# Optimization experiments

Measured on AMD Instinct MI355X. Metric: run time of the kernel, lower is better.

The kernel has to match this reference:

```python
import jax, jax.numpy as jnp
import numpy as np

B, S, DIN = 4, 2048, 1024
H, D = 16, 64  # num_head, per-head dim_out


def _xavier(key, shape):
    fan_in, fan_out = shape[0], shape[1]
    limit = float(np.sqrt(6.0 / (fan_in + fan_out)))
    return jax.random.uniform(key, shape, jnp.float32, -limit, limit)


def setup_inputs() -> dict:
    key = jax.random.key(0)
    k_x, k_q, k_k, k_v, k_o = jax.random.split(key, 5)
    inputs = jax.random.normal(k_x, (B, S, DIN), jnp.float32)
    # weights stored as [in, out] (transpose of torch Linear.weight); bias zeros
    return {
        "inputs": inputs,
        "wq": _xavier(k_q, (DIN, H * D)), "bq": jnp.zeros((H * D,), jnp.float32),
        "wk": _xavier(k_k, (DIN, H * D)), "bk": jnp.zeros((H * D,), jnp.float32),
        "wv": _xavier(k_v, (DIN, H * D)), "bv": jnp.zeros((H * D,), jnp.float32),
        "wo": _xavier(k_o, (H * D, D)),  "bo": jnp.zeros((D,), jnp.float32),
    }


def reference(inputs, wq, bq, wk, bk, wv, bv, wo, bo):
    b, s, _ = inputs.shape
    q = (inputs @ wq + bq).reshape(b, s, H, D).transpose(0, 2, 1, 3)  # bhsd
    k = (inputs @ wk + bk).reshape(b, s, H, D).transpose(0, 2, 1, 3)
    v = (inputs @ wv + bv).reshape(b, s, H, D).transpose(0, 2, 1, 3)
    scores = jnp.einsum('bhsd,bhSd->bhsS', q, k) / jnp.sqrt(jnp.float32(D))
    p = jax.nn.softmax(scores, axis=-1)
    o = jnp.einsum('bhsS,bhSd->bhsd', p, v)
    o = o.transpose(0, 2, 1, 3).reshape(b, s, H * D)
    return o @ wo + bo  # [b, s, D]
```

## Files before the change

kernel.cpp:

```cpp
#include <hip/hip_runtime.h>

typedef __attribute__((ext_vector_type(8))) __bf16 bf16x8;
typedef __attribute__((ext_vector_type(4))) float f32x4;

#define NB   4
#define NS   2048
#define NDIN 1024
#define NH   16
#define ND   64
#define NHD  1024
#define NM   (NB * NS)

__device__ __forceinline__ float bf2f(unsigned short u) {
    unsigned int x = ((unsigned int)u) << 16;
    return __builtin_bit_cast(float, x);
}
__device__ __forceinline__ unsigned short f2bf(float f) {
    unsigned int u = __builtin_bit_cast(unsigned int, f);
    u += 0x7fff + ((u >> 16) & 1);
    return (unsigned short)(u >> 16);
}
__device__ __forceinline__ unsigned int cvt_pk_bf16(float lo, float hi) {
    unsigned int r;
    asm("v_cvt_pk_bf16_f32 %0, %1, %2" : "=v"(r) : "v"(lo), "v"(hi));
    return r;
}
__device__ __forceinline__ void gload16(const unsigned short* g, unsigned short* l) {
    __builtin_amdgcn_global_load_lds((const __attribute__((address_space(1))) unsigned int*)g,
                                     (__attribute__((address_space(3))) unsigned int*)l, 16, 0, 0);
}

__global__ __launch_bounds__(256) void cvt_x(const float* __restrict__ src,
                                             unsigned short* __restrict__ dst) {
    int i = blockIdx.x * 256 + threadIdx.x;
    float4 a = ((const float4*)src)[i * 2];
    float4 b = ((const float4*)src)[i * 2 + 1];
    union { uint4 u; unsigned short s[8]; } o;
    o.s[0] = f2bf(a.x); o.s[1] = f2bf(a.y); o.s[2] = f2bf(a.z); o.s[3] = f2bf(a.w);
    o.s[4] = f2bf(b.x); o.s[5] = f2bf(b.y); o.s[6] = f2bf(b.z); o.s[7] = f2bf(b.w);
    *(uint4*)(dst + (size_t)i * 8) = o.u;
}

__global__ void transpose_cvt3(const float* __restrict__ wq, const float* __restrict__ wk,
                               const float* __restrict__ wv, unsigned short* __restrict__ dst_all) {
    __shared__ unsigned short t[32][33];
    const float* src = blockIdx.z == 0 ? wq : blockIdx.z == 1 ? wk : wv;
    unsigned short* dst = dst_all + (size_t)blockIdx.z * 1024 * 1024;
    int k0 = blockIdx.x * 32, n0 = blockIdx.y * 32;
    int tx = threadIdx.x, ty = threadIdx.y;
#pragma unroll
    for (int i = 0; i < 32; i += 8)
        t[ty + i][tx] = f2bf(src[(size_t)(k0 + ty + i) * 1024 + (n0 + tx)]);
    __syncthreads();
#pragma unroll
    for (int i = 0; i < 32; i += 8)
        dst[(size_t)(n0 + ty + i) * 1024 + (k0 + tx)] = t[tx][ty + i];
}

__global__ void transpose_cvt(const float* __restrict__ src,
                              unsigned short* __restrict__ dst, int K, int N) {
    __shared__ unsigned short t[32][33];
    int k0 = blockIdx.x * 32, n0 = blockIdx.y * 32;
    int tx = threadIdx.x, ty = threadIdx.y;
#pragma unroll
    for (int i = 0; i < 32; i += 8)
        t[ty + i][tx] = f2bf(src[(size_t)(k0 + ty + i) * N + (n0 + tx)]);
    __syncthreads();
#pragma unroll
    for (int i = 0; i < 32; i += 8)
        dst[(size_t)(n0 + ty + i) * K + (k0 + tx)] = t[tx][ty + i];
}

__global__ __launch_bounds__(256) void gemm_qkv(
    const unsigned short* __restrict__ X, const unsigned short* __restrict__ Wt,
    const float* __restrict__ bq, const float* __restrict__ bk,
    const float* __restrict__ bv,
    unsigned short* __restrict__ Q, unsigned short* __restrict__ K,
    unsigned short* __restrict__ V) {
    __shared__ unsigned short smem[128 * 128];
    unsigned short (*Al)[32] = (unsigned short (*)[32])smem;
    unsigned short (*Bl)[32] = (unsigned short (*)[32])(smem + 128 * 32);
    unsigned short (*Cl)[128] = (unsigned short (*)[128])smem;

    int lin = blockIdx.x;
    int xcd = lin & 7, ii = lin >> 3;
    int mt = xcd * 8 + (ii & 7);
    int nt = ii >> 3;
    int mb = mt * 128, nb = nt * 128;

    int tid = threadIdx.x;
    int wid = tid >> 6, lane = tid & 63, quad = lane >> 4, l16 = lane & 15;
    int wm = (wid & 1) * 64, wn = (wid >> 1) * 64;

    int srow = 16 * wid + (lane >> 2);
    int scol = (lane & 3) * 8;
    const unsigned short* pa0 = X + (size_t)(mb + srow) * NDIN + scol;
    const unsigned short* pa1 = pa0 + (size_t)64 * NDIN;
    const unsigned short* pb0 = Wt + (size_t)(nb + srow) * NDIN + scol;
    const unsigned short* pb1 = pb0 + (size_t)64 * NDIN;
    unsigned short* la = smem + wid * 512;
    unsigned short* lb = smem + 128 * 32 + wid * 512;

    f32x4 acc[4][4];
#pragma unroll
    for (int i = 0; i < 4; i++)
#pragma unroll
        for (int j = 0; j < 4; j++) acc[i][j] = (f32x4){0.f, 0.f, 0.f, 0.f};

    for (int k0 = 0; k0 < NDIN; k0 += 32) {
        gload16(pa0, la);
        gload16(pa1, la + 2048);
        gload16(pb0, lb);
        gload16(pb1, lb + 2048);
        pa0 += 32; pa1 += 32; pb0 += 32; pb1 += 32;
        __syncthreads();
        bf16x8 af[4], bfr[4];
#pragma unroll
        for (int i = 0; i < 4; i++)
            af[i] = *(const bf16x8*)(&Al[wm + i * 16 + l16][quad * 8]);
#pragma unroll
        for (int j = 0; j < 4; j++)
            bfr[j] = *(const bf16x8*)(&Bl[wn + j * 16 + l16][quad * 8]);
#pragma unroll
        for (int i = 0; i < 4; i++)
#pragma unroll
            for (int j = 0; j < 4; j++)
                acc[i][j] = __builtin_amdgcn_mfma_f32_16x16x32_bf16(af[i], bfr[j], acc[i][j], 0, 0, 0);
        __syncthreads();
    }

    int wsel = nb >> 10;
    const float* bias = (wsel == 0) ? bq : (wsel == 1) ? bk : bv;
    unsigned short* dstp = (wsel == 0) ? Q : (wsel == 1) ? K : V;
#pragma unroll
    for (int i = 0; i < 4; i++)
#pragma unroll
        for (int j = 0; j < 4; j++) {
            int nl = wn + j * 16 + l16;
            float bias_v = bias[(nb & 1023) + nl];
#pragma unroll
            for (int r = 0; r < 4; r++) {
                int ml = wm + i * 16 + quad * 4 + r;
                int pc = ((nl >> 3) ^ (ml & 15));
                Cl[ml][(pc << 3) | (nl & 7)] = f2bf(acc[i][j][r] + bias_v);
            }
        }
    __syncthreads();
    {
        int hl = tid >> 7, sl = tid & 127;
        int h = ((nb & 1023) >> 6) + hl;
        int m = mb + sl, b = m >> 11, sidx = m & 2047;
        unsigned short* orow = dstp + ((size_t)((b * NH + h) * NS + sidx)) * ND;
#pragma unroll
        for (int c = 0; c < 8; c++) {
            int pc = ((hl * 8 + c) ^ (sl & 15));
            *(uint4*)(orow + c * 8) = *(const uint4*)(&Cl[sl][pc << 3]);
        }
    }
}

__global__ __launch_bounds__(256) void attn(
    const unsigned short* __restrict__ Q, const unsigned short* __restrict__ K,
    const unsigned short* __restrict__ V, unsigned short* __restrict__ Obuf) {
    __shared__ unsigned short Kl[2][64][64];
    __shared__ unsigned short Vt[2][64][64];

    int lin = blockIdx.x;
    int xcd = lin & 7, idx = lin >> 3;
    int bh = ((idx >> 4) << 3) | xcd;
    int qt = idx & 15;

    size_t base = (size_t)bh * NS * ND;
    int tid = threadIdx.x, wid = tid >> 6, lane = tid & 63;
    int quad = lane >> 4, l16 = lane & 15;
    int lx = l16 & 7;
    int q0 = qt * 128 + wid * 32;

    bf16x8 qa[2][2];
#pragma unroll
    for (int s = 0; s < 2; s++)
#pragma unroll
        for (int f = 0; f < 2; f++) {
            union { uint4 u; unsigned short sv[8]; } in_, out_;
            in_.u = *(const uint4*)(Q + base + (size_t)(q0 + s * 16 + l16) * ND + f * 32 + quad * 8);
#pragma unroll
            for (int j = 0; j < 8; j++) out_.sv[j] = f2bf(bf2f(in_.sv[j]) * 0.125f);
            qa[s][f] = __builtin_bit_cast(bf16x8, out_.u);
        }

    float lrow[2] = {0.f, 0.f};
    f32x4 o[2][4];
#pragma unroll
    for (int s = 0; s < 2; s++)
#pragma unroll
        for (int t = 0; t < 4; t++) o[s][t] = (f32x4){0.f, 0.f, 0.f, 0.f};

    int c0 = tid, c1 = tid + 256;
    int kr0w = c0 >> 3, kc0 = c0 & 7, kg0c = kc0 ^ (kr0w & 7);
    int kr1w = c1 >> 3, kc1 = c1 & 7, kg1c = kc1 ^ (kr1w & 7);
    const unsigned short* kp0 = K + base + (size_t)kr0w * ND + kc0 * 8;
    const unsigned short* kp1 = K + base + (size_t)kr1w * ND + kc1 * 8;
    int p = tid & 31, dqA = tid >> 5, dqB = dqA + 8;
    int cp = ((p >> 4) << 2) | ((p >> 1) & 3);
    int ps = (((p >> 3) & 1) << 2) | ((p & 1) << 1);
    int cb = cp ^ ((dqA & 1) << 2);
    const unsigned short* vg = V + base + (size_t)(2 * p) * ND + dqA * 4;

    uint4 k0r, k1r;
    uint2 va0, va1, va2, va3;

    auto writeKV = [&](int buf) {
        *(uint4*)(&Kl[buf][kr0w][kg0c * 8]) = k0r;
        *(uint4*)(&Kl[buf][kr1w][kg1c * 8]) = k1r;
        unsigned short* vt = &Vt[buf][0][0];
        unsigned int w0 = __builtin_amdgcn_perm(va1.x, va0.x, 0x05040100u);
        unsigned int w1 = __builtin_amdgcn_perm(va1.x, va0.x, 0x07060302u);
        unsigned int w2 = __builtin_amdgcn_perm(va1.y, va0.y, 0x05040100u);
        unsigned int w3 = __builtin_amdgcn_perm(va1.y, va0.y, 0x07060302u);
        *(unsigned int*)(vt + (dqA * 4 + 0) * 64 + ((cb ^ 0) << 3) + ps) = w0;
        *(unsigned int*)(vt + (dqA * 4 + 1) * 64 + ((cb ^ 1) << 3) + ps) = w1;
        *(unsigned int*)(vt + (dqA * 4 + 2) * 64 + ((cb ^ 2) << 3) + ps) = w2;
        *(unsigned int*)(vt + (dqA * 4 + 3) * 64 + ((cb ^ 3) << 3) + ps) = w3;
        unsigned int x0 = __builtin_amdgcn_perm(va3.x, va2.x, 0x05040100u);
        unsigned int x1 = __builtin_amdgcn_perm(va3.x, va2.x, 0x07060302u);
        unsigned int x2 = __builtin_amdgcn_perm(va3.y, va2.y, 0x05040100u);
        unsigned int x3 = __builtin_amdgcn_perm(va3.y, va2.y, 0x07060302u);
        *(unsigned int*)(vt + (dqB * 4 + 0) * 64 + ((cb ^ 0) << 3) + ps) = x0;
        *(unsigned int*)(vt + (dqB * 4 + 1) * 64 + ((cb ^ 1) << 3) + ps) = x1;
        *(unsigned int*)(vt + (dqB * 4 + 2) * 64 + ((cb ^ 2) << 3) + ps) = x2;
        *(unsigned int*)(vt + (dqB * 4 + 3) * 64 + ((cb ^ 3) << 3) + ps) = x3;
    };

    k0r = *(const uint4*)kp0;
    k1r = *(const uint4*)kp1;
    va0 = *(const uint2*)(vg);
    va1 = *(const uint2*)(vg + ND);
    va2 = *(const uint2*)(vg + 32);
    va3 = *(const uint2*)(vg + ND + 32);
    writeKV(0);
    __syncthreads();

    int cur = 0;
    for (int kc = 0; kc < NS; kc += 64) {
        bool more = (kc + 64 < NS);
        if (more) {
            kp0 += 64 * ND; kp1 += 64 * ND; vg += 64 * ND;
            k0r = *(const uint4*)kp0;
            k1r = *(const uint4*)kp1;
            va0 = *(const uint2*)(vg);
            va1 = *(const uint2*)(vg + ND);
            va2 = *(const uint2*)(vg + 32);
            va3 = *(const uint2*)(vg + ND + 32);
        }

        const unsigned short (*Kc)[64] = Kl[cur];
        const unsigned short (*Vc)[64] = Vt[cur];

        f32x4 st[2][4];
        __builtin_amdgcn_s_setprio(1);
#pragma unroll
        for (int sub = 0; sub < 4; sub++) {
            bf16x8 kb0 = *(const bf16x8*)(&Kc[sub * 16 + l16][((quad ^ lx) << 3)]);
            bf16x8 kb1 = *(const bf16x8*)(&Kc[sub * 16 + l16][(((4 + quad) ^ lx) << 3)]);
#pragma unroll
            for (int s = 0; s < 2; s++) {
                f32x4 c = (f32x4){0.f, 0.f, 0.f, 0.f};
                c = __builtin_amdgcn_mfma_f32_16x16x32_bf16(kb0, qa[s][0], c, 0, 0, 0);
                c = __builtin_amdgcn_mfma_f32_16x16x32_bf16(kb1, qa[s][1], c, 0, 0, 0);
                st[s][sub] = c;
            }
        }
        __builtin_amdgcn_s_setprio(0);

        bf16x8 pb[2][2];
#pragma unroll
        for (int s = 0; s < 2; s++) {
            float sum = 0.f;
#pragma unroll
            for (int sub = 0; sub < 4; sub++)
#pragma unroll
                for (int r = 0; r < 4; r++) {
                    float pv = __expf(st[s][sub][r]);
                    st[s][sub][r] = pv;
                    sum += pv;
                }
            lrow[s] += sum;
            unsigned int a0 = cvt_pk_bf16(st[s][0][0], st[s][0][1]);
            unsigned int a1 = cvt_pk_bf16(st[s][0][2], st[s][0][3]);
            unsigned int a2 = cvt_pk_bf16(st[s][1][0], st[s][1][1]);
            unsigned int a3 = cvt_pk_bf16(st[s][1][2], st[s][1][3]);
            pb[s][0] = __builtin_bit_cast(bf16x8, (uint4){a0, a1, a2, a3});
            unsigned int b0 = cvt_pk_bf16(st[s][2][0], st[s][2][1]);
            unsigned int b1 = cvt_pk_bf16(st[s][2][2], st[s][2][3]);
            unsigned int b2 = cvt_pk_bf16(st[s][3][0], st[s][3][1]);
            unsigned int b3 = cvt_pk_bf16(st[s][3][2], st[s][3][3]);
            pb[s][1] = __builtin_bit_cast(bf16x8, (uint4){b0, b1, b2, b3});
        }

        __builtin_amdgcn_s_setprio(1);
#pragma unroll
        for (int t = 0; t < 4; t++) {
            bf16x8 vb0 = *(const bf16x8*)(&Vc[t * 16 + l16][((quad ^ lx) << 3)]);
            bf16x8 vb1 = *(const bf16x8*)(&Vc[t * 16 + l16][(((4 + quad) ^ lx) << 3)]);
#pragma unroll
            for (int s = 0; s < 2; s++) {
                o[s][t] = __builtin_amdgcn_mfma_f32_16x16x32_bf16(vb0, pb[s][0], o[s][t], 0, 0, 0);
                o[s][t] = __builtin_amdgcn_mfma_f32_16x16x32_bf16(vb1, pb[s][1], o[s][t], 0, 0, 0);
            }
        }
        __builtin_amdgcn_s_setprio(0);

        if (more) {
            int nxt = cur ^ 1;
            writeKV(nxt);
            __syncthreads();
            cur = nxt;
        }
    }

    int b = bh >> 4, h = bh & 15;
#pragma unroll
    for (int s = 0; s < 2; s++) {
        float ls = lrow[s];
        ls += __shfl_xor(ls, 16, 64);
        ls += __shfl_xor(ls, 32, 64);
        float inv = 1.0f / ls;
        int q = q0 + s * 16 + l16;
#pragma unroll
        for (int t = 0; t < 4; t++) {
            uint2 w;
            w.x = cvt_pk_bf16(o[s][t][0] * inv, o[s][t][1] * inv);
            w.y = cvt_pk_bf16(o[s][t][2] * inv, o[s][t][3] * inv);
            *(uint2*)(Obuf + (size_t)(b * NS + q) * NHD + h * ND + t * 16 + quad * 4) = w;
        }
    }
}

__global__ __launch_bounds__(256) void out_proj(
    const unsigned short* __restrict__ Obuf, const unsigned short* __restrict__ WoT,
    const float* __restrict__ bo, float* __restrict__ Out) {
    __shared__ float red[4][16][64];
    int m0 = blockIdx.x * 16;
    int tid = threadIdx.x, wid = tid >> 6, lane = tid & 63;
    int quad = lane >> 4, l16 = lane & 15;
    f32x4 acc[4];
#pragma unroll
    for (int t = 0; t < 4; t++) acc[t] = (f32x4){0.f, 0.f, 0.f, 0.f};
    int kb = wid * 256;
    for (int k0 = kb; k0 < kb + 256; k0 += 32) {
        bf16x8 a = *(const bf16x8*)(Obuf + (size_t)(m0 + l16) * NHD + k0 + quad * 8);
#pragma unroll
        for (int t = 0; t < 4; t++) {
            bf16x8 b = *(const bf16x8*)(WoT + (size_t)(t * 16 + l16) * NHD + k0 + quad * 8);
            acc[t] = __builtin_amdgcn_mfma_f32_16x16x32_bf16(a, b, acc[t], 0, 0, 0);
        }
    }
#pragma unroll
    for (int t = 0; t < 4; t++)
#pragma unroll
        for (int r = 0; r < 4; r++) red[wid][t * 4 + r][lane] = acc[t][r];
    __syncthreads();
    if (tid < 64) {
        int q2 = tid >> 4, s16 = tid & 15;
#pragma unroll
        for (int t = 0; t < 4; t++) {
            int n = t * 16 + s16;
            float bb = bo[n];
#pragma unroll
            for (int r = 0; r < 4; r++) {
                int idx = t * 4 + r;
                float v = red[0][idx][tid] + red[1][idx][tid] + red[2][idx][tid] + red[3][idx][tid];
                int m = m0 + q2 * 4 + r;
                Out[(size_t)m * ND + n] = v + bb;
            }
        }
    }
}

extern "C" void kernel_launch(void* const* d_in, const int* in_sizes, int n_in,
                              void* d_out, int out_size, void* d_ws, size_t ws_size,
                              hipStream_t stream) {
    const float* X  = (const float*)d_in[0];
    const float* wq = (const float*)d_in[1];
    const float* bq = (const float*)d_in[2];
    const float* wk = (const float*)d_in[3];
    const float* bk = (const float*)d_in[4];
    const float* wv = (const float*)d_in[5];
    const float* bv = (const float*)d_in[6];
    const float* wo = (const float*)d_in[7];
    const float* bo = (const float*)d_in[8];
    float* Out = (float*)d_out;

    char* w = (char*)d_ws;
    unsigned short* Wt  = (unsigned short*)w; w += (size_t)3072 * 1024 * 2;
    unsigned short* WoT = (unsigned short*)w; w += (size_t)64 * 1024 * 2;
    unsigned short* Xb  = (unsigned short*)w; w += (size_t)NM * NDIN * 2;
    unsigned short* Qb  = (unsigned short*)w; w += (size_t)NM * NHD * 2;
    unsigned short* Kb  = (unsigned short*)w; w += (size_t)NM * NHD * 2;
    unsigned short* Vb  = (unsigned short*)w; w += (size_t)NM * NHD * 2;
    unsigned short* Ob  = (unsigned short*)w; w += (size_t)NM * NHD * 2;

    cvt_x<<<NM * NDIN / (256 * 8), 256, 0, stream>>>(X, Xb);

    dim3 tb(32, 8);
    transpose_cvt3<<<dim3(32, 32, 3), tb, 0, stream>>>(wq, wk, wv, Wt);
    transpose_cvt<<<dim3(32, 2), tb, 0, stream>>>(wo, WoT, 1024, 64);

    gemm_qkv<<<1536, 256, 0, stream>>>(Xb, Wt, bq, bk, bv, Qb, Kb, Vb);
    attn<<<1024, 256, 0, stream>>>(Qb, Kb, Vb, Ob);
    out_proj<<<512, 256, 0, stream>>>(Ob, WoT, bo, Out);
}
```

Measured before the change: 277.4 us.

## Merge prep kernels, double-buffer QKV GEMM LDS, software-pipeline attention loop

Merges the three fp32-to-bf16 conversion and transpose kernels into one launch that dispatches by block index. The QKV GEMM gains a second LDS buffer so the next K-slice load is issued before the MFMAs on the current one, removing one barrier per iteration. The attention loop is restructured so that QK^T for the next block and PV for the current block are interleaved, with softmax done outside the high-priority region and K/V staged two blocks ahead. This trades more registers (two P fragment sets) and a second barrier per attention iteration for more overlap of global loads and MFMA work.

```diff
diff --git a/kernel.cpp b/kernel.cpp
--- a/kernel.cpp
+++ b/kernel.cpp
@@ -30,45 +30,47 @@
                                      (__attribute__((address_space(3))) unsigned int*)l, 16, 0, 0);
 }
 
-__global__ __launch_bounds__(256) void cvt_x(const float* __restrict__ src,
-                                             unsigned short* __restrict__ dst) {
-    int i = blockIdx.x * 256 + threadIdx.x;
-    float4 a = ((const float4*)src)[i * 2];
-    float4 b = ((const float4*)src)[i * 2 + 1];
-    union { uint4 u; unsigned short s[8]; } o;
-    o.s[0] = f2bf(a.x); o.s[1] = f2bf(a.y); o.s[2] = f2bf(a.z); o.s[3] = f2bf(a.w);
-    o.s[4] = f2bf(b.x); o.s[5] = f2bf(b.y); o.s[6] = f2bf(b.z); o.s[7] = f2bf(b.w);
-    *(uint4*)(dst + (size_t)i * 8) = o.u;
-}
-
-__global__ void transpose_cvt3(const float* __restrict__ wq, const float* __restrict__ wk,
-                               const float* __restrict__ wv, unsigned short* __restrict__ dst_all) {
+__global__ __launch_bounds__(256) void prep(
+    const float* __restrict__ X, const float* __restrict__ wq,
+    const float* __restrict__ wk, const float* __restrict__ wv,
+    const float* __restrict__ wo, unsigned short* __restrict__ Xb,
+    unsigned short* __restrict__ Wt, unsigned short* __restrict__ WoT) {
     __shared__ unsigned short t[32][33];
-    const float* src = blockIdx.z == 0 ? wq : blockIdx.z == 1 ? wk : wv;
-    unsigned short* dst = dst_all + (size_t)blockIdx.z * 1024 * 1024;
-    int k0 = blockIdx.x * 32, n0 = blockIdx.y * 32;
-    int tx = threadIdx.x, ty = threadIdx.y;
-#pragma unroll
-    for (int i = 0; i < 32; i += 8)
-        t[ty + i][tx] = f2bf(src[(size_t)(k0 + ty + i) * 1024 + (n0 + tx)]);
-    __syncthreads();
-#pragma unroll
-    for (int i = 0; i < 32; i += 8)
-        dst[(size_t)(n0 + ty + i) * 1024 + (k0 + tx)] = t[tx][ty + i];
-}
-
-__global__ void transpose_cvt(const float* __restrict__ src,
-                              unsigned short* __restrict__ dst, int K, int N) {
-    __shared__ unsigned short t[32][33];
-    int k0 = blockIdx.x * 32, n0 = blockIdx.y * 32;
-    int tx = threadIdx.x, ty = threadIdx.y;
-#pragma unroll
-    for (int i = 0; i < 32; i += 8)
-        t[ty + i][tx] = f2bf(src[(size_t)(k0 + ty + i) * N + (n0 + tx)]);
-    __syncthreads();
-#pragma unroll
-    for (int i = 0; i < 32; i += 8)
-        dst[(size_t)(n0 + ty + i) * K + (k0 + tx)] = t[tx][ty + i];
+    int blk = blockIdx.x, tid = threadIdx.x;
+    if (blk < 4096) {
+        int i = blk * 256 + tid;
+        float4 a = ((const float4*)X)[i * 2];
+        float4 b = ((const float4*)X)[i * 2 + 1];
+        union { uint4 u; unsigned short s[8]; } o;
+        o.s[0] = f2bf(a.x); o.s[1] = f2bf(a.y); o.s[2] = f2bf(a.z); o.s[3] = f2bf(a.w);
+        o.s[4] = f2bf(b.x); o.s[5] = f2bf(b.y); o.s[6] = f2bf(b.z); o.s[7] = f2bf(b.w);
+        *(uint4*)(Xb + (size_t)i * 8) = o.u;
+    } else if (blk < 4096 + 3072) {
+        int bb = blk - 4096;
+        int z = bb >> 10, rem = bb & 1023;
+        const float* src = z == 0 ? wq : z == 1 ? wk : wv;
+        unsigned short* dst = Wt + (size_t)z * 1024 * 1024;
+        int k0 = (rem & 31) * 32, n0 = (rem >> 5) * 32;
+        int tx = tid & 31, ty = tid >> 5;
+#pragma unroll
+        for (int i = 0; i < 32; i += 8)
+            t[ty + i][tx] = f2bf(src[(size_t)(k0 + ty + i) * 1024 + (n0 + tx)]);
+        __syncthreads();
+#pragma unroll
+        for (int i = 0; i < 32; i += 8)
+            dst[(size_t)(n0 + ty + i) * 1024 + (k0 + tx)] = t[tx][ty + i];
+    } else {
+        int bb = blk - 7168;
+        int k0 = (bb & 31) * 32, n0 = (bb >> 5) * 32;
+        int tx = tid & 31, ty = tid >> 5;
+#pragma unroll
+        for (int i = 0; i < 32; i += 8)
+            t[ty + i][tx] = f2bf(wo[(size_t)(k0 + ty + i) * 64 + (n0 + tx)]);
+        __syncthreads();
+#pragma unroll
+        for (int i = 0; i < 32; i += 8)
+            WoT[(size_t)(n0 + ty + i) * 1024 + (k0 + tx)] = t[tx][ty + i];
+    }
 }
 
 __global__ __launch_bounds__(256) void gemm_qkv(
@@ -77,10 +79,7 @@
     const float* __restrict__ bv,
     unsigned short* __restrict__ Q, unsigned short* __restrict__ K,
     unsigned short* __restrict__ V) {
-    __shared__ unsigned short smem[128 * 128];
-    unsigned short (*Al)[32] = (unsigned short (*)[32])smem;
-    unsigned short (*Bl)[32] = (unsigned short (*)[32])(smem + 128 * 32);
-    unsigned short (*Cl)[128] = (unsigned short (*)[128])smem;
+    __shared__ unsigned short smem[16384];
 
     int lin = blockIdx.x;
     int xcd = lin & 7, ii = lin >> 3;
@@ -98,37 +97,47 @@
     const unsigned short* pa1 = pa0 + (size_t)64 * NDIN;
     const unsigned short* pb0 = Wt + (size_t)(nb + srow) * NDIN + scol;
     const unsigned short* pb1 = pb0 + (size_t)64 * NDIN;
-    unsigned short* la = smem + wid * 512;
-    unsigned short* lb = smem + 128 * 32 + wid * 512;
-
-    f32x4 acc[4][4];
-#pragma unroll
-    for (int i = 0; i < 4; i++)
-#pragma unroll
-        for (int j = 0; j < 4; j++) acc[i][j] = (f32x4){0.f, 0.f, 0.f, 0.f};
-
-    for (int k0 = 0; k0 < NDIN; k0 += 32) {
+
+    auto stage = [&](int buf) {
+        unsigned short* la = smem + buf * 8192 + wid * 512;
+        unsigned short* lb = smem + buf * 8192 + 4096 + wid * 512;
         gload16(pa0, la);
         gload16(pa1, la + 2048);
         gload16(pb0, lb);
         gload16(pb1, lb + 2048);
         pa0 += 32; pa1 += 32; pb0 += 32; pb1 += 32;
-        __syncthreads();
+    };
+
+    f32x4 acc[4][4];
+#pragma unroll
+    for (int i = 0; i < 4; i++)
+#pragma unroll
+        for (int j = 0; j < 4; j++) acc[i][j] = (f32x4){0.f, 0.f, 0.f, 0.f};
+
+    stage(0);
+    __syncthreads();
+    int cur = 0;
+    for (int k0 = 0; k0 < NDIN; k0 += 32) {
+        if (k0 + 32 < NDIN) stage(cur ^ 1);
+        const unsigned short* Ab = smem + cur * 8192;
+        const unsigned short* Bb = Ab + 4096;
         bf16x8 af[4], bfr[4];
 #pragma unroll
         for (int i = 0; i < 4; i++)
-            af[i] = *(const bf16x8*)(&Al[wm + i * 16 + l16][quad * 8]);
+            af[i] = *(const bf16x8*)(Ab + (wm + i * 16 + l16) * 32 + quad * 8);
 #pragma unroll
         for (int j = 0; j < 4; j++)
-            bfr[j] = *(const bf16x8*)(&Bl[wn + j * 16 + l16][quad * 8]);
+            bfr[j] = *(const bf16x8*)(Bb + (wn + j * 16 + l16) * 32 + quad * 8);
 #pragma unroll
         for (int i = 0; i < 4; i++)
 #pragma unroll
             for (int j = 0; j < 4; j++)
                 acc[i][j] = __builtin_amdgcn_mfma_f32_16x16x32_bf16(af[i], bfr[j], acc[i][j], 0, 0, 0);
         __syncthreads();
-    }
-
+        cur ^= 1;
+    }
+
+    unsigned short (*Cl)[128] = (unsigned short (*)[128])smem;
     int wsel = nb >> 10;
     const float* bias = (wsel == 0) ? bq : (wsel == 1) ? bk : bv;
     unsigned short* dstp = (wsel == 0) ? Q : (wsel == 1) ? K : V;
@@ -208,6 +217,16 @@
 
     uint4 k0r, k1r;
     uint2 va0, va1, va2, va3;
+
+    auto loadRegs = [&]() {
+        k0r = *(const uint4*)kp0;
+        k1r = *(const uint4*)kp1;
+        va0 = *(const uint2*)(vg);
+        va1 = *(const uint2*)(vg + ND);
+        va2 = *(const uint2*)(vg + 32);
+        va3 = *(const uint2*)(vg + ND + 32);
+    };
+    auto bump = [&]() { kp0 += 64 * ND; kp1 += 64 * ND; vg += 64 * ND; };
 
     auto writeKV = [&](int buf) {
         *(uint4*)(&Kl[buf][kr0w][kg0c * 8]) = k0r;
@@ -231,37 +250,14 @@
         *(unsigned int*)(vt + (dqB * 4 + 3) * 64 + ((cb ^ 3) << 3) + ps) = x3;
     };
 
-    k0r = *(const uint4*)kp0;
-    k1r = *(const uint4*)kp1;
-    va0 = *(const uint2*)(vg);
-    va1 = *(const uint2*)(vg + ND);
-    va2 = *(const uint2*)(vg + 32);
-    va3 = *(const uint2*)(vg + ND + 32);
-    writeKV(0);
-    __syncthreads();
-
-    int cur = 0;
-    for (int kc = 0; kc < NS; kc += 64) {
-        bool more = (kc + 64 < NS);
-        if (more) {
-            kp0 += 64 * ND; kp1 += 64 * ND; vg += 64 * ND;
-            k0r = *(const uint4*)kp0;
-            k1r = *(const uint4*)kp1;
-            va0 = *(const uint2*)(vg);
-            va1 = *(const uint2*)(vg + ND);
-            va2 = *(const uint2*)(vg + 32);
-            va3 = *(const uint2*)(vg + ND + 32);
-        }
-
-        const unsigned short (*Kc)[64] = Kl[cur];
-        const unsigned short (*Vc)[64] = Vt[cur];
-
-        f32x4 st[2][4];
-        __builtin_amdgcn_s_setprio(1);
+    f32x4 st[2][4];
+    bf16x8 pbA[2][2], pbB[2][2];
+
+    auto QKT = [&](int nb_) {
 #pragma unroll
         for (int sub = 0; sub < 4; sub++) {
-            bf16x8 kb0 = *(const bf16x8*)(&Kc[sub * 16 + l16][((quad ^ lx) << 3)]);
-            bf16x8 kb1 = *(const bf16x8*)(&Kc[sub * 16 + l16][(((4 + quad) ^ lx) << 3)]);
+            bf16x8 kb0 = *(const bf16x8*)(&Kl[nb_][sub * 16 + l16][((quad ^ lx) << 3)]);
+            bf16x8 kb1 = *(const bf16x8*)(&Kl[nb_][sub * 16 + l16][(((4 + quad) ^ lx) << 3)]);
 #pragma unroll
             for (int s = 0; s < 2; s++) {
                 f32x4 c = (f32x4){0.f, 0.f, 0.f, 0.f};
@@ -270,9 +266,8 @@
                 st[s][sub] = c;
             }
         }
-        __builtin_amdgcn_s_setprio(0);
-
-        bf16x8 pb[2][2];
+    };
+    auto SM = [&](bf16x8 (&pbP)[2][2]) {
 #pragma unroll
         for (int s = 0; s < 2; s++) {
             float sum = 0.f;
@@ -289,34 +284,55 @@
             unsigned int a1 = cvt_pk_bf16(st[s][0][2], st[s][0][3]);
             unsigned int a2 = cvt_pk_bf16(st[s][1][0], st[s][1][1]);
             unsigned int a3 = cvt_pk_bf16(st[s][1][2], st[s][1][3]);
-            pb[s][0] = __builtin_bit_cast(bf16x8, (uint4){a0, a1, a2, a3});
+            pbP[s][0] = __builtin_bit_cast(bf16x8, (uint4){a0, a1, a2, a3});
             unsigned int b0 = cvt_pk_bf16(st[s][2][0], st[s][2][1]);
             unsigned int b1 = cvt_pk_bf16(st[s][2][2], st[s][2][3]);
             unsigned int b2 = cvt_pk_bf16(st[s][3][0], st[s][3][1]);
             unsigned int b3 = cvt_pk_bf16(st[s][3][2], st[s][3][3]);
-            pb[s][1] = __builtin_bit_cast(bf16x8, (uint4){b0, b1, b2, b3});
-        }
-
+            pbP[s][1] = __builtin_bit_cast(bf16x8, (uint4){b0, b1, b2, b3});
+        }
+    };
+    auto PV = [&](int cb_, bf16x8 (&pbC)[2][2]) {
+#pragma unroll
+        for (int t = 0; t < 4; t++) {
+            bf16x8 vb0 = *(const bf16x8*)(&Vt[cb_][t * 16 + l16][((quad ^ lx) << 3)]);
+            bf16x8 vb1 = *(const bf16x8*)(&Vt[cb_][t * 16 + l16][(((4 + quad) ^ lx) << 3)]);
+#pragma unroll
+            for (int s = 0; s < 2; s++) {
+                o[s][t] = __builtin_amdgcn_mfma_f32_16x16x32_bf16(vb0, pbC[s][0], o[s][t], 0, 0, 0);
+                o[s][t] = __builtin_amdgcn_mfma_f32_16x16x32_bf16(vb1, pbC[s][1], o[s][t], 0, 0, 0);
+            }
+        }
+    };
+
+    auto body = [&](int cb_, int nb_, bf16x8 (&pbC)[2][2], bf16x8 (&pbP)[2][2], bool more) {
+        if (more) { bump(); loadRegs(); }
         __builtin_amdgcn_s_setprio(1);
-#pragma unroll
-        for (int t = 0; t < 4; t++) {
-            bf16x8 vb0 = *(const bf16x8*)(&Vc[t * 16 + l16][((quad ^ lx) << 3)]);
-            bf16x8 vb1 = *(const bf16x8*)(&Vc[t * 16 + l16][(((4 + quad) ^ lx) << 3)]);
-#pragma unroll
-            for (int s = 0; s < 2; s++) {
-                o[s][t] = __builtin_amdgcn_mfma_f32_16x16x32_bf16(vb0, pb[s][0], o[s][t], 0, 0, 0);
-                o[s][t] = __builtin_amdgcn_mfma_f32_16x16x32_bf16(vb1, pb[s][1], o[s][t], 0, 0, 0);
-            }
-        }
+        QKT(nb_);
+        PV(cb_, pbC);
         __builtin_amdgcn_s_setprio(0);
-
-        if (more) {
-            int nxt = cur ^ 1;
-            writeKV(nxt);
-            __syncthreads();
-            cur = nxt;
-        }
-    }
+        SM(pbP);
+        __syncthreads();
+        if (more) writeKV(cb_);
+        __syncthreads();
+    };
+
+    loadRegs();
+    writeKV(0);
+    bump(); loadRegs();
+    writeKV(1);
+    __syncthreads();
+    QKT(0);
+    SM(pbA);
+
+    for (int it = 0; it < 15; ++it) {
+        body(0, 1, pbA, pbB, true);
+        body(1, 0, pbB, pbA, true);
+    }
+    body(0, 1, pbA, pbB, false);
+    __builtin_amdgcn_s_setprio(1);
+    PV(1, pbB);
+    __builtin_amdgcn_s_setprio(0);
 
     int b = bh >> 4, h = bh & 15;
 #pragma unroll
@@ -400,12 +416,7 @@
     unsigned short* Vb  = (unsigned short*)w; w += (size_t)NM * NHD * 2;
     unsigned short* Ob  = (unsigned short*)w; w += (size_t)NM * NHD * 2;
 
-    cvt_x<<<NM * NDIN / (256 * 8), 256, 0, stream>>>(X, Xb);
-
-    dim3 tb(32, 8);
-    transpose_cvt3<<<dim3(32, 32, 3), tb, 0, stream>>>(wq, wk, wv, Wt);
-    transpose_cvt<<<dim3(32, 2), tb, 0, stream>>>(wo, WoT, 1024, 64);
-
+    prep<<<7232, 256, 0, stream>>>(X, wq, wk, wv, wo, Xb, Wt, WoT);
     gemm_qkv<<<1536, 256, 0, stream>>>(Xb, Wt, bq, bk, bv, Qb, Kb, Vb);
     attn<<<1024, 256, 0, stream>>>(Qb, Kb, Vb, Ob);
     out_proj<<<512, 256, 0, stream>>>(Ob, WoT, bo, Out);
```

New measurement: 272.7 us. Within noise of the previous version (-1.7%).
